# Kernel optimization log

Hardware: AMD Instinct MI355X
Metric: run time of the kernel (lower is better)

Reference implementation:

```python
import jax, jax.numpy as jnp
import numpy as np

BS, IN_F, OUT_F = 1024, 128, 100000
M, S, ALPHA = 0.35, 30.0, 0.5


def _l2norm(x):
    # F.normalize: x / max(||x||, eps)
    n = jnp.sqrt(jnp.sum(x * x, axis=-1, keepdims=True))
    return x / jnp.maximum(n, 1e-12)


def setup_inputs() -> dict:
    key = jax.random.key(0)
    k1, k2, k3 = jax.random.split(key, 3)
    return {
        "input": jax.random.normal(k1, (BS, IN_F), dtype=jnp.float32),
        "label": jax.random.randint(k2, (BS,), 0, OUT_F, dtype=jnp.int64),
        "weight": jax.random.normal(k3, (OUT_F, IN_F), dtype=jnp.float32),
    }


def reference(input, label, weight):
    wn = _l2norm(weight)                      # [nc, d]
    fn = _l2norm(input)                       # [bs, d]
    logits = jnp.einsum('bd,cd->bc', fn, wn)  # [bs, nc] cosine sims
    bs = fn.shape[0]
    rows = jnp.arange(bs)

    pos = jnp.take_along_axis(logits, label[:, None], axis=1)[:, 0] * S  # [bs]
    # negatives: all classes except the label (replaces masked_select + view)
    neg = (logits * S).at[rows, label].set(-jnp.inf)
    lse_neg = jax.nn.logsumexp(neg, axis=1)   # [bs]

    # loss = mean(log(1 + exp(m + lse_neg - pos)))
    loss = jnp.mean(jax.nn.softplus(M + lse_neg - pos))

    # weight.data update: per-class mean of normalized features for classes
    # present in the batch (the torch loop is exactly a segment-mean; note
    # weight_update aliases weight.data so the final blend is a no-op and the
    # result is simply: present rows <- class mean, other rows unchanged).
    sums = jax.ops.segment_sum(fn, label, num_segments=OUT_F)                # [nc, d]
    counts = jax.ops.segment_sum(jnp.ones((bs,), fn.dtype), label, num_segments=OUT_F)
    present = counts > 0
    class_mean = sums / jnp.maximum(counts, 1.0)[:, None]
    new_weight = jnp.where(present[:, None], class_mean, weight)

    return loss, new_weight
```

## Files before the change

### kernel.cpp

```cpp
#include <hip/hip_runtime.h>

#define BS 1024
#define D 128
#define NC 100000
#define NCP 100096
#define NT64 1564
#define PHASES 256
#define S_SCALE 30.0f
#define MARGIN 0.35f
#define S2LOG2E 43.2808512f

typedef __attribute__((ext_vector_type(8))) short bf16x8;
typedef __attribute__((ext_vector_type(4))) float f32x4;

__device__ __forceinline__ unsigned short f2bf(float f) {
    union { float f; unsigned u; } x; x.f = f;
    unsigned u = x.u;
    u += 0x7FFFu + ((u >> 16) & 1u);
    return (unsigned short)(u >> 16);
}


__global__ void prep_fn(const float* __restrict__ inp, const int* __restrict__ label,
                        const float* __restrict__ wt,
                        float* __restrict__ fn_f32, unsigned short* __restrict__ fn_fr,
                        float* __restrict__ counts, float* __restrict__ pos) {
    int row = blockIdx.x * 4 + (threadIdx.x >> 6);
    int lane = threadIdx.x & 63;
    float2 v = *(const float2*)(inp + row * D + lane * 2);
    float s = v.x * v.x + v.y * v.y;
    #pragma unroll
    for (int m = 1; m < 64; m <<= 1) s += __shfl_xor(s, m);
    float inv = 1.0f / fmaxf(sqrtf(s), 1e-12f);
    float a = v.x * inv, b = v.y * inv;
    *(float2*)(fn_f32 + row * D + lane * 2) = make_float2(a, b);
    unsigned pack = (unsigned)f2bf(a) | ((unsigned)f2bf(b) << 16);
    ((unsigned*)fn_fr)[(row >> 4) * 1024 + (lane >> 2) * 64 + ((row & 15) << 2) + (lane & 3)] = pack;

    int c = label[row];
    float2 wv = *(const float2*)(wt + c * D + lane * 2);
    float sw_ = wv.x * wv.x + wv.y * wv.y;
    float dt  = wv.x * a + wv.y * b;
    #pragma unroll
    for (int m = 1; m < 64; m <<= 1) { sw_ += __shfl_xor(sw_, m); dt += __shfl_xor(dt, m); }
    if (lane == 0) {
        float invw = 1.0f / fmaxf(sqrtf(sw_), 1e-12f);
        pos[row] = S_SCALE * dt * invw;
        atomicAdd(counts + c, 1.0f);
    }
}

#define LOADV()  do {                                                         \
    if (rg < NC) {                                                            \
        const float* p_ = wt + (size_t)rg * 128 + 2 * g16;                    \
        v0 = *(const float2*)(p_);      v1 = *(const float2*)(p_ + 32);       \
        v2 = *(const float2*)(p_ + 64); v3 = *(const float2*)(p_ + 96);       \
    } else { v0 = v1 = v2 = v3 = make_float2(0.f, 0.f); }                     \
} while (0)

#define COMMIT(buf) do {                                                      \
    float ss = v0.x*v0.x + v0.y*v0.y + v1.x*v1.x + v1.y*v1.y                  \
             + v2.x*v2.x + v2.y*v2.y + v3.x*v3.x + v3.y*v3.y;                 \
    ss += __shfl_xor(ss, 1); ss += __shfl_xor(ss, 2);                         \
    ss += __shfl_xor(ss, 4); ss += __shfl_xor(ss, 8);                         \
    float inv = 1.0f / fmaxf(sqrtf(ss), 1e-12f);                              \
    unsigned* Wu_ = (unsigned*)(buf);                                         \
    int base_ = (rloc >> 4) * 1024 + (g16 >> 2) * 64 + (rloc & 15) * 4 + (g16 & 3); \
    Wu_[base_]       = (unsigned)f2bf(v0.x*inv) | ((unsigned)f2bf(v0.y*inv) << 16); \
    Wu_[base_ + 256] = (unsigned)f2bf(v1.x*inv) | ((unsigned)f2bf(v1.y*inv) << 16); \
    Wu_[base_ + 512] = (unsigned)f2bf(v2.x*inv) | ((unsigned)f2bf(v2.y*inv) << 16); \
    Wu_[base_ + 768] = (unsigned)f2bf(v3.x*inv) | ((unsigned)f2bf(v3.y*inv) << 16); \
    if (writeout && rg < NC) {                                                \
        float cnt_ = counts[rg];                                              \
        float* op_ = outw + (size_t)rg * 128 + 2 * g16;                       \
        float2 z_ = make_float2(0.f, 0.f);                                    \
        *(float2*)(op_)      = (cnt_ > 0.f) ? z_ : v0;                        \
        *(float2*)(op_ + 32) = (cnt_ > 0.f) ? z_ : v1;                        \
        *(float2*)(op_ + 64) = (cnt_ > 0.f) ? z_ : v2;                        \
        *(float2*)(op_ + 96) = (cnt_ > 0.f) ? z_ : v3;                        \
    }                                                                         \
} while (0)

__global__ __launch_bounds__(1024, 4) void main_gemm(
    const unsigned short* __restrict__ fnfr, const float* __restrict__ wt,
    const float* __restrict__ counts, float* __restrict__ sumexp,
    float* __restrict__ outw) {
    __shared__ __align__(16) short Ws[2][8192];
    const int tid = threadIdx.x;
    const int lane = tid & 63, w = tid >> 6;
    const int g16 = tid & 15;
    const int rloc = tid >> 4;
    const int half = blockIdx.y;
    const bool writeout = (half == 0);

    bf16x8 bf[2][4];
    {
        const char* gB = (const char*)fnfr + (size_t)(half * 32 + w * 2) * 4096 + lane * 16;
        #pragma unroll
        for (int cg = 0; cg < 2; cg++)
            #pragma unroll
            for (int ks = 0; ks < 4; ks++)
                bf[cg][ks] = *(const bf16x8*)(gB + cg * 4096 + ks * 1024);
    }
    #pragma unroll
    for (int cg = 0; cg < 2; cg++)
        #pragma unroll
        for (int ks = 0; ks < 4; ks++)
            asm volatile("" : "+v"(bf[cg][ks]));

    float sums[2] = {0.0f, 0.0f};
    float2 v0, v1, v2, v3;

    int rg = blockIdx.x * 64 + rloc;
    LOADV();
    COMMIT(Ws[0]);
    __syncthreads();

    int cur = 0;
    for (int t = blockIdx.x; t < NT64; t += PHASES) {
        int nxt = t + PHASES;
        if (nxt < NT64) { rg = nxt * 64 + rloc; LOADV(); }

        f32x4 acc[4][2];
        #pragma unroll
        for (int ag = 0; ag < 4; ag++)
            #pragma unroll
            for (int cg = 0; cg < 2; cg++)
                acc[ag][cg] = (f32x4){0.0f, 0.0f, 0.0f, 0.0f};

        const char* W = (const char*)Ws[cur];
        #pragma unroll
        for (int ks = 0; ks < 4; ks++) {
            bf16x8 a0 = *(const bf16x8*)(W +     0 + ks * 1024 + lane * 16);
            bf16x8 a1 = *(const bf16x8*)(W +  4096 + ks * 1024 + lane * 16);
            bf16x8 a2 = *(const bf16x8*)(W +  8192 + ks * 1024 + lane * 16);
            bf16x8 a3 = *(const bf16x8*)(W + 12288 + ks * 1024 + lane * 16);
            acc[0][0] = __builtin_amdgcn_mfma_f32_16x16x32_bf16(a0, bf[0][ks], acc[0][0], 0, 0, 0);
            acc[0][1] = __builtin_amdgcn_mfma_f32_16x16x32_bf16(a0, bf[1][ks], acc[0][1], 0, 0, 0);
            acc[1][0] = __builtin_amdgcn_mfma_f32_16x16x32_bf16(a1, bf[0][ks], acc[1][0], 0, 0, 0);
            acc[1][1] = __builtin_amdgcn_mfma_f32_16x16x32_bf16(a1, bf[1][ks], acc[1][1], 0, 0, 0);
            acc[2][0] = __builtin_amdgcn_mfma_f32_16x16x32_bf16(a2, bf[0][ks], acc[2][0], 0, 0, 0);
            acc[2][1] = __builtin_amdgcn_mfma_f32_16x16x32_bf16(a2, bf[1][ks], acc[2][1], 0, 0, 0);
            acc[3][0] = __builtin_amdgcn_mfma_f32_16x16x32_bf16(a3, bf[0][ks], acc[3][0], 0, 0, 0);
            acc[3][1] = __builtin_amdgcn_mfma_f32_16x16x32_bf16(a3, bf[1][ks], acc[3][1], 0, 0, 0);
        }

        #pragma unroll
        for (int ag = 0; ag < 4; ag++)
            #pragma unroll
            for (int r = 0; r < 4; r++) {
                sums[0] += __builtin_amdgcn_exp2f(fmaf(acc[ag][0][r], S2LOG2E, -S2LOG2E));
                sums[1] += __builtin_amdgcn_exp2f(fmaf(acc[ag][1][r], S2LOG2E, -S2LOG2E));
            }

        if (nxt < NT64) COMMIT(Ws[cur ^ 1]);
        __syncthreads();
        cur ^= 1;
    }

    #pragma unroll
    for (int cg = 0; cg < 2; cg++) {
        float s = sums[cg];
        s += __shfl_xor(s, 16);
        s += __shfl_xor(s, 32);
        if (lane < 16)
            atomicAdd(sumexp + half * 512 + w * 32 + cg * 16 + lane, s);
    }
}

__global__ void tail_k(const float* __restrict__ fn_f32, const int* __restrict__ label,
                       const float* __restrict__ counts, float* __restrict__ outw,
                       const float* __restrict__ sumexp, const float* __restrict__ pos,
                       float* __restrict__ out) {
    if (blockIdx.x < 512) {
        int b = blockIdx.x * 2 + (threadIdx.x >> 7);
        int t = threadIdx.x & 127;
        int c = label[b];
        atomicAdd(outw + (size_t)c * D + t, fn_f32[b * D + t] / counts[c]);
        return;
    }
    __shared__ float red[256];
    int t = threadIdx.x;
    float acc = 0.0f;
    #pragma unroll
    for (int i = 0; i < 4; i++) {
        int r = t + i * 256;
        float p = pos[r];
        float sneg = fmaxf(sumexp[r] - __expf(p - 30.0f), 1e-38f);
        float lse = 30.0f + logf(sneg);
        float z = MARGIN + lse - p;
        acc += fmaxf(z, 0.0f) + log1pf(__expf(-fabsf(z)));
    }
    red[t] = acc;
    __syncthreads();
    for (int s = 128; s > 0; s >>= 1) {
        if (t < s) red[t] += red[t + s];
        __syncthreads();
    }
    if (t == 0) out[0] = red[0] * (1.0f / 1024.0f);
}

extern "C" void kernel_launch(void* const* d_in, const int* in_sizes, int n_in,
                              void* d_out, int out_size, void* d_ws, size_t ws_size,
                              hipStream_t stream) {
    (void)in_sizes; (void)n_in; (void)out_size; (void)ws_size;
    const float* inp   = (const float*)d_in[0];
    const int*   label = (const int*)d_in[1];
    const float* wt    = (const float*)d_in[2];
    float* out = (float*)d_out;

    char* w = (char*)d_ws;
    float*          fn_f32 = (float*)(w);
    unsigned short* fn_fr  = (unsigned short*)(w + 524288);
    float*          sumexp = (float*)(w + 26411008);
    float*          counts = (float*)(w + 26415104);
    float*          pos    = (float*)(w + 26815104);

    hipMemsetAsync(w + 26411008, 0, 404096, stream);

    prep_fn<<<BS / 4, 256, 0, stream>>>(inp, label, wt, fn_f32, fn_fr, counts, pos);
    main_gemm<<<dim3(PHASES, 2), 1024, 0, stream>>>(fn_fr, wt, counts, sumexp, out + 1);
    tail_k<<<513, 256, 0, stream>>>(fn_f32, label, counts, out + 1, sumexp, pos, out);
}
```

Measured before the change: 139.3 us.

## Halve GEMM block to 512 threads with more batch columns per wave

Main GEMM blocks drop from 1024 to 512 threads. Each wave now holds 4 batch column groups of fn in registers instead of 2, and each thread loads 8 float2 per weight row instead of 4. The MFMA loop is split into four passes over A-groups, with the next tile's global load placed after the first pass so it overlaps compute. bf16 packing now uses the hardware v_cvt_pk_bf16_f32 instruction instead of manual rounding. This cuts per-thread accumulator pressure and normalisation cost, at the price of more registers held for B fragments and fewer threads to hide latency.

```diff
diff --git a/kernel.cpp b/kernel.cpp
--- a/kernel.cpp
+++ b/kernel.cpp
@@ -13,11 +13,19 @@
 typedef __attribute__((ext_vector_type(8))) short bf16x8;
 typedef __attribute__((ext_vector_type(4))) float f32x4;
 
+#define MFMA(a, b, c) __builtin_amdgcn_mfma_f32_16x16x32_bf16((a), (b), (c), 0, 0, 0)
+
 __device__ __forceinline__ unsigned short f2bf(float f) {
     union { float f; unsigned u; } x; x.f = f;
     unsigned u = x.u;
     u += 0x7FFFu + ((u >> 16) & 1u);
     return (unsigned short)(u >> 16);
+}
+
+__device__ __forceinline__ unsigned pkbf(float lo, float hi) {
+    unsigned r;
+    asm("v_cvt_pk_bf16_f32 %0, %1, %2" : "=v"(r) : "v"(lo), "v"(hi));
+    return r;
 }
 
 
@@ -50,66 +58,94 @@
     }
 }
 
-#define LOADV()  do {                                                         \
+#define LOADV() do {                                                          \
     if (rg < NC) {                                                            \
-        const float* p_ = wt + (size_t)rg * 128 + 2 * g16;                    \
-        v0 = *(const float2*)(p_);      v1 = *(const float2*)(p_ + 32);       \
-        v2 = *(const float2*)(p_ + 64); v3 = *(const float2*)(p_ + 96);       \
-    } else { v0 = v1 = v2 = v3 = make_float2(0.f, 0.f); }                     \
+        const float2* p_ = (const float2*)(wt + (size_t)rg * 128) + g8;       \
+        v0 = p_[0];  v1 = p_[8];  v2 = p_[16]; v3 = p_[24];                   \
+        v4 = p_[32]; v5 = p_[40]; v6 = p_[48]; v7 = p_[56];                   \
+    } else {                                                                  \
+        v0 = v1 = v2 = v3 = v4 = v5 = v6 = v7 = make_float2(0.f, 0.f);        \
+    }                                                                         \
 } while (0)
 
 #define COMMIT(buf) do {                                                      \
     float ss = v0.x*v0.x + v0.y*v0.y + v1.x*v1.x + v1.y*v1.y                  \
-             + v2.x*v2.x + v2.y*v2.y + v3.x*v3.x + v3.y*v3.y;                 \
-    ss += __shfl_xor(ss, 1); ss += __shfl_xor(ss, 2);                         \
-    ss += __shfl_xor(ss, 4); ss += __shfl_xor(ss, 8);                         \
+             + v2.x*v2.x + v2.y*v2.y + v3.x*v3.x + v3.y*v3.y                  \
+             + v4.x*v4.x + v4.y*v4.y + v5.x*v5.x + v5.y*v5.y                  \
+             + v6.x*v6.x + v6.y*v6.y + v7.x*v7.x + v7.y*v7.y;                 \
+    ss += __shfl_xor(ss, 1); ss += __shfl_xor(ss, 2); ss += __shfl_xor(ss, 4);\
     float inv = 1.0f / fmaxf(sqrtf(ss), 1e-12f);                              \
     unsigned* Wu_ = (unsigned*)(buf);                                         \
-    int base_ = (rloc >> 4) * 1024 + (g16 >> 2) * 64 + (rloc & 15) * 4 + (g16 & 3); \
-    Wu_[base_]       = (unsigned)f2bf(v0.x*inv) | ((unsigned)f2bf(v0.y*inv) << 16); \
-    Wu_[base_ + 256] = (unsigned)f2bf(v1.x*inv) | ((unsigned)f2bf(v1.y*inv) << 16); \
-    Wu_[base_ + 512] = (unsigned)f2bf(v2.x*inv) | ((unsigned)f2bf(v2.y*inv) << 16); \
-    Wu_[base_ + 768] = (unsigned)f2bf(v3.x*inv) | ((unsigned)f2bf(v3.y*inv) << 16); \
+    int b_ = (rloc >> 4) * 1024 + (g8 >> 2) * 64 + (rloc & 15) * 4 + (g8 & 3);\
+    Wu_[b_      ] = pkbf(v0.x * inv, v0.y * inv);                             \
+    Wu_[b_ + 128] = pkbf(v1.x * inv, v1.y * inv);                             \
+    Wu_[b_ + 256] = pkbf(v2.x * inv, v2.y * inv);                             \
+    Wu_[b_ + 384] = pkbf(v3.x * inv, v3.y * inv);                             \
+    Wu_[b_ + 512] = pkbf(v4.x * inv, v4.y * inv);                             \
+    Wu_[b_ + 640] = pkbf(v5.x * inv, v5.y * inv);                             \
+    Wu_[b_ + 768] = pkbf(v6.x * inv, v6.y * inv);                             \
+    Wu_[b_ + 896] = pkbf(v7.x * inv, v7.y * inv);                             \
     if (writeout && rg < NC) {                                                \
         float cnt_ = counts[rg];                                              \
-        float* op_ = outw + (size_t)rg * 128 + 2 * g16;                       \
+        float2* op_ = (float2*)(outw + (size_t)rg * 128) + g8;                \
         float2 z_ = make_float2(0.f, 0.f);                                    \
-        *(float2*)(op_)      = (cnt_ > 0.f) ? z_ : v0;                        \
-        *(float2*)(op_ + 32) = (cnt_ > 0.f) ? z_ : v1;                        \
-        *(float2*)(op_ + 64) = (cnt_ > 0.f) ? z_ : v2;                        \
-        *(float2*)(op_ + 96) = (cnt_ > 0.f) ? z_ : v3;                        \
+        op_[0]  = cnt_ > 0.f ? z_ : v0;  op_[8]  = cnt_ > 0.f ? z_ : v1;      \
+        op_[16] = cnt_ > 0.f ? z_ : v2;  op_[24] = cnt_ > 0.f ? z_ : v3;      \
+        op_[32] = cnt_ > 0.f ? z_ : v4;  op_[40] = cnt_ > 0.f ? z_ : v5;      \
+        op_[48] = cnt_ > 0.f ? z_ : v6;  op_[56] = cnt_ > 0.f ? z_ : v7;      \
     }                                                                         \
 } while (0)
 
-__global__ __launch_bounds__(1024, 4) void main_gemm(
+#define PASS(ag) do {                                                         \
+    const char* W_ = (const char*)Ws[cur] + (ag) * 4096 + lane * 16;          \
+    f32x4 c0 = (f32x4){0,0,0,0}, c1 = (f32x4){0,0,0,0};                       \
+    f32x4 c2 = (f32x4){0,0,0,0}, c3 = (f32x4){0,0,0,0};                       \
+    _Pragma("unroll")                                                         \
+    for (int ks = 0; ks < 4; ks++) {                                          \
+        bf16x8 a_ = *(const bf16x8*)(W_ + ks * 1024);                         \
+        c0 = MFMA(a_, bf[0][ks], c0);                                         \
+        c1 = MFMA(a_, bf[1][ks], c1);                                         \
+        c2 = MFMA(a_, bf[2][ks], c2);                                         \
+        c3 = MFMA(a_, bf[3][ks], c3);                                         \
+    }                                                                         \
+    _Pragma("unroll")                                                         \
+    for (int r = 0; r < 4; r++) {                                             \
+        sums[0] += __builtin_amdgcn_exp2f(fmaf(c0[r], S2LOG2E, -S2LOG2E));    \
+        sums[1] += __builtin_amdgcn_exp2f(fmaf(c1[r], S2LOG2E, -S2LOG2E));    \
+        sums[2] += __builtin_amdgcn_exp2f(fmaf(c2[r], S2LOG2E, -S2LOG2E));    \
+        sums[3] += __builtin_amdgcn_exp2f(fmaf(c3[r], S2LOG2E, -S2LOG2E));    \
+    }                                                                         \
+} while (0)
+
+__global__ __launch_bounds__(512, 4) void main_gemm(
     const unsigned short* __restrict__ fnfr, const float* __restrict__ wt,
     const float* __restrict__ counts, float* __restrict__ sumexp,
     float* __restrict__ outw) {
     __shared__ __align__(16) short Ws[2][8192];
     const int tid = threadIdx.x;
     const int lane = tid & 63, w = tid >> 6;
-    const int g16 = tid & 15;
-    const int rloc = tid >> 4;
-    const int half = blockIdx.y;
-    const bool writeout = (half == 0);
-
-    bf16x8 bf[2][4];
+    const int g8 = tid & 7;
+    const int rloc = tid >> 3;
+    const int slice = blockIdx.y;
+    const bool writeout = (slice == 0);
+
+    bf16x8 bf[4][4];
     {
-        const char* gB = (const char*)fnfr + (size_t)(half * 32 + w * 2) * 4096 + lane * 16;
+        const char* gB = (const char*)fnfr + (size_t)(slice * 32 + w * 4) * 4096 + lane * 16;
         #pragma unroll
-        for (int cg = 0; cg < 2; cg++)
+        for (int cg = 0; cg < 4; cg++)
             #pragma unroll
             for (int ks = 0; ks < 4; ks++)
                 bf[cg][ks] = *(const bf16x8*)(gB + cg * 4096 + ks * 1024);
     }
     #pragma unroll
-    for (int cg = 0; cg < 2; cg++)
+    for (int cg = 0; cg < 4; cg++)
         #pragma unroll
         for (int ks = 0; ks < 4; ks++)
             asm volatile("" : "+v"(bf[cg][ks]));
 
-    float sums[2] = {0.0f, 0.0f};
-    float2 v0, v1, v2, v3;
+    float sums[4] = {0.0f, 0.0f, 0.0f, 0.0f};
+    float2 v0, v1, v2, v3, v4, v5, v6, v7;
 
     int rg = blockIdx.x * 64 + rloc;
     LOADV();
@@ -119,52 +155,23 @@
     int cur = 0;
     for (int t = blockIdx.x; t < NT64; t += PHASES) {
         int nxt = t + PHASES;
+        PASS(0);
         if (nxt < NT64) { rg = nxt * 64 + rloc; LOADV(); }
-
-        f32x4 acc[4][2];
-        #pragma unroll
-        for (int ag = 0; ag < 4; ag++)
-            #pragma unroll
-            for (int cg = 0; cg < 2; cg++)
-                acc[ag][cg] = (f32x4){0.0f, 0.0f, 0.0f, 0.0f};
-
-        const char* W = (const char*)Ws[cur];
-        #pragma unroll
-        for (int ks = 0; ks < 4; ks++) {
-            bf16x8 a0 = *(const bf16x8*)(W +     0 + ks * 1024 + lane * 16);
-            bf16x8 a1 = *(const bf16x8*)(W +  4096 + ks * 1024 + lane * 16);
-            bf16x8 a2 = *(const bf16x8*)(W +  8192 + ks * 1024 + lane * 16);
-            bf16x8 a3 = *(const bf16x8*)(W + 12288 + ks * 1024 + lane * 16);
-            acc[0][0] = __builtin_amdgcn_mfma_f32_16x16x32_bf16(a0, bf[0][ks], acc[0][0], 0, 0, 0);
-            acc[0][1] = __builtin_amdgcn_mfma_f32_16x16x32_bf16(a0, bf[1][ks], acc[0][1], 0, 0, 0);
-            acc[1][0] = __builtin_amdgcn_mfma_f32_16x16x32_bf16(a1, bf[0][ks], acc[1][0], 0, 0, 0);
-            acc[1][1] = __builtin_amdgcn_mfma_f32_16x16x32_bf16(a1, bf[1][ks], acc[1][1], 0, 0, 0);
-            acc[2][0] = __builtin_amdgcn_mfma_f32_16x16x32_bf16(a2, bf[0][ks], acc[2][0], 0, 0, 0);
-            acc[2][1] = __builtin_amdgcn_mfma_f32_16x16x32_bf16(a2, bf[1][ks], acc[2][1], 0, 0, 0);
-            acc[3][0] = __builtin_amdgcn_mfma_f32_16x16x32_bf16(a3, bf[0][ks], acc[3][0], 0, 0, 0);
-            acc[3][1] = __builtin_amdgcn_mfma_f32_16x16x32_bf16(a3, bf[1][ks], acc[3][1], 0, 0, 0);
-        }
-
-        #pragma unroll
-        for (int ag = 0; ag < 4; ag++)
-            #pragma unroll
-            for (int r = 0; r < 4; r++) {
-                sums[0] += __builtin_amdgcn_exp2f(fmaf(acc[ag][0][r], S2LOG2E, -S2LOG2E));
-                sums[1] += __builtin_amdgcn_exp2f(fmaf(acc[ag][1][r], S2LOG2E, -S2LOG2E));
-            }
-
+        PASS(1);
+        PASS(2);
+        PASS(3);
         if (nxt < NT64) COMMIT(Ws[cur ^ 1]);
         __syncthreads();
         cur ^= 1;
     }
 
     #pragma unroll
-    for (int cg = 0; cg < 2; cg++) {
+    for (int cg = 0; cg < 4; cg++) {
         float s = sums[cg];
         s += __shfl_xor(s, 16);
         s += __shfl_xor(s, 32);
         if (lane < 16)
-            atomicAdd(sumexp + half * 512 + w * 32 + cg * 16 + lane, s);
+            atomicAdd(sumexp + slice * 512 + w * 64 + cg * 16 + lane, s);
     }
 }
 
@@ -219,6 +226,6 @@
     hipMemsetAsync(w + 26411008, 0, 404096, stream);
 
     prep_fn<<<BS / 4, 256, 0, stream>>>(inp, label, wt, fn_f32, fn_fr, counts, pos);
-    main_gemm<<<dim3(PHASES, 2), 1024, 0, stream>>>(fn_fr, wt, counts, sumexp, out + 1);
+    main_gemm<<<dim3(PHASES, 2), 512, 0, stream>>>(fn_fr, wt, counts, sumexp, out + 1);
     tail_k<<<513, 256, 0, stream>>>(fn_f32, label, counts, out + 1, sumexp, pos, out);
 }
```

Measured after the change: 297.5 us. 114% more time.
